# Performance work log

Hardware: AMD Instinct MI355X
Metric: run time of the kernel (lower is better)

The kernel has to match this reference:

```python
import math
import jax, jax.numpy as jnp
import numpy as np

N_HEADS = 16

def _alibi_slopes(n_heads: int) -> np.ndarray:
    def pow2_slopes(n):
        start = 2 ** (-2 ** (-(math.log2(n) - 3)))
        return [start * start ** i for i in range(n)]
    if math.log2(n_heads).is_integer():
        slopes = pow2_slopes(n_heads)
    else:
        closest = 2 ** math.floor(math.log2(n_heads))
        slopes = pow2_slopes(closest)
        extra = pow2_slopes(2 * closest)[0::2]
        slopes = slopes + extra[: n_heads - closest]
    return np.asarray(slopes, dtype=np.float32)

def _build_alibi_bias(n_heads: int, T: int) -> jnp.ndarray:
    # (1, H, T, T): lower triangle = -slope*|i-j|, strict upper = -inf (causal)
    slopes = jnp.asarray(_alibi_slopes(n_heads))  # (H,)
    pos = jnp.arange(T)
    dist = pos[None, :] - pos[None, :].T  # (T, T), j - i
    causal = dist < 0  # future positions (j > i means dist>0? note: dist = j - i transposed)
    # match torch: distances = positions[None,:] - positions[:,None] -> dist[i,j] = j - i
    dist = pos[None, :] - pos[:, None]
    causal = dist > 0  # wait: torch masks distances < 0 where distances[i,j] = j - i? No:
    # torch: distances = positions.unsqueeze(0) - positions.unsqueeze(1) -> dist[i,j] = positions[j] - positions[i]? 
    # unsqueeze(0): (1,T) row j; unsqueeze(1): (T,1) row i -> dist[i,j] = pos[j] - pos[i]
    # causal_mask = dist < 0 masks j < i ... but then bias upper triangle kept?
    # Actually torch masks where distances < 0, i.e., j < i (past). That seems inverted,
    # but we must be FAITHFUL: mask fills -inf where pos[j] - pos[i] < 0.
    d = pos[None, :] - pos[:, None]  # d[i,j] = j - i
    mask = d < 0
    bias = -slopes[:, None, None] * jnp.abs(d).astype(jnp.float32)[None, :, :]
    bias = jnp.where(mask[None, :, :], -jnp.inf, bias)
    return bias[None]  # (1, H, T, T)

def setup_inputs() -> dict:
    key = jax.random.key(0)
    k1, k2, k3 = jax.random.split(key, 3)
    B, T, D = 2, 2048, 1024
    x = jax.random.normal(k1, (B, T, D), dtype=jnp.float32)
    W_qkv = jax.random.normal(k2, (D, 3 * D), dtype=jnp.float32) * (1.0 / math.sqrt(D))
    W_out = jax.random.normal(k3, (D, D), dtype=jnp.float32) * (1.0 / math.sqrt(D))
    return {"x": x, "W_qkv": W_qkv, "W_out": W_out}

def reference(x, W_qkv, W_out):
    B, T, D = x.shape
    H = N_HEADS
    hd = D // H
    qkv = x @ W_qkv  # (B, T, 3D)
    q, k, v = jnp.split(qkv, 3, axis=-1)
    q = q.reshape(B, T, H, hd).transpose(0, 2, 1, 3)  # (B,H,T,hd)
    k = k.reshape(B, T, H, hd).transpose(0, 2, 1, 3)
    v = v.reshape(B, T, H, hd).transpose(0, 2, 1, 3)
    scale = 1.0 / math.sqrt(hd)
    attn = jnp.einsum('bhqd,bhkd->bhqk', q, k) * scale  # (B,H,T,T)
    attn = attn + _build_alibi_bias(H, T)
    attn = jax.nn.softmax(attn, axis=-1)
    out = jnp.einsum('bhqk,bhkd->bhqd', attn, v)  # (B,H,T,hd)
    out = out.transpose(0, 2, 1, 3).reshape(B, T, D)
    return out @ W_out
```

## Files before the change

kernel.cpp:

```cpp
#include <hip/hip_runtime.h>

#define DEV __device__ __forceinline__

typedef __attribute__((ext_vector_type(4))) float f32x4;
typedef __attribute__((ext_vector_type(16))) float f32x16;
typedef __attribute__((ext_vector_type(8))) short s16x8;

static constexpr int TB  = 2;
static constexpr int TT  = 2048;
static constexpr int TD  = 1024;
static constexpr int TH  = 16;
static constexpr int THD = 64;
static constexpr int TN3 = 3072;
static constexpr int TM  = TB * TT;

#define WS_XB     1024u
#define WS_WQKVT  (WS_XB + 8388608u)
#define WS_WOUTT  (WS_WQKVT + 6291456u)
#define WS_QKV    (WS_WOUTT + 2097152u)
#define WS_VT     (WS_QKV + 25165824u)
#define WS_CTX    (WS_VT + 8388608u)

DEV unsigned short f2bf(float f) {
  unsigned int u = __builtin_bit_cast(unsigned int, f);
  u += 0x7FFFu + ((u >> 16) & 1u);
  return (unsigned short)(u >> 16);
}
DEV f32x4 mfma16(s16x8 a, s16x8 b, f32x4 c) {
  return __builtin_amdgcn_mfma_f32_16x16x32_bf16(a, b, c, 0, 0, 0);
}
DEV f32x16 mfma32(s16x8 a, s16x8 b, f32x16 c) {
  return __builtin_amdgcn_mfma_f32_32x32x16_bf16(a, b, c, 0, 0, 0);
}
DEV void gload_lds16(const void* g, void* l) {
  __builtin_amdgcn_global_load_lds(
      (const __attribute__((address_space(1))) void*)g,
      (__attribute__((address_space(3))) void*)l, 16, 0, 0);
}
DEV unsigned int cvtpk(float lo, float hi_) {
  unsigned int r;
  asm("v_cvt_pk_bf16_f32 %0, %1, %2" : "=v"(r) : "v"(lo), "v"(hi_));
  return r;
}
DEV void plswap(unsigned int& a, unsigned int& b) {
  asm("v_permlane32_swap_b32 %0, %1" : "+v"(a), "+v"(b));
}

DEV bool is_bf16(const void* x) {
  uint4 v = ((const uint4*)x)[threadIdx.x & 63];
  unsigned int w[4] = {v.x, v.y, v.z, v.w};
  int hit = 0;
#pragma unroll
  for (int k = 0; k < 4; ++k) {
    if (((w[k] >> 7) & 0xFF) >= 135) hit++;
    if (((w[k] >> 23) & 0xFF) >= 135) hit++;
  }
  return __ballot(hit > 0) == 0ULL;
}

__global__ __launch_bounds__(256) void prep_kernel(const void* __restrict__ x,
                                                   const void* __restrict__ wqkv,
                                                   const void* __restrict__ wout,
                                                   unsigned short* __restrict__ xb,
                                                   unsigned short* __restrict__ wqkvt,
                                                   unsigned short* __restrict__ woutt) {
  __shared__ unsigned short tile[64 * 65];
  const int bid = blockIdx.x;
  const bool bf = is_bf16(x);
  if (bid < 1024) {
    const void* W; unsigned short* Wt; int N, k0, n0;
    if (bid < 768) { W = wqkv; Wt = wqkvt; N = TN3; k0 = (bid & 15) * 64; n0 = (bid >> 4) * 64; }
    else { int id = bid - 768; W = wout; Wt = woutt; N = TD; k0 = (id & 15) * 64; n0 = (id >> 4) * 64; }
    for (int e = threadIdx.x; e < 4096; e += 256) {
      int kr = e >> 6, nc = e & 63;
      unsigned short v;
      if (bf) v = ((const unsigned short*)W)[(size_t)(k0 + kr) * N + n0 + nc];
      else    v = f2bf(((const float*)W)[(size_t)(k0 + kr) * N + n0 + nc]);
      tile[kr * 65 + nc] = v;
    }
    __syncthreads();
    for (int e = threadIdx.x; e < 4096; e += 256) {
      int nr = e >> 6, kc = e & 63;
      Wt[(size_t)(n0 + nr) * TD + k0 + kc] = tile[kc * 65 + nr];
    }
  } else {
    if (bf) return;
    int i = (bid - 1024) * 256 + threadIdx.x;
    if (i >= (TM * TD) / 8) return;
    const float* s = (const float*)x + (size_t)i * 8;
    unsigned int w0 = (unsigned int)f2bf(s[0]) | ((unsigned int)f2bf(s[1]) << 16);
    unsigned int w1 = (unsigned int)f2bf(s[2]) | ((unsigned int)f2bf(s[3]) << 16);
    unsigned int w2 = (unsigned int)f2bf(s[4]) | ((unsigned int)f2bf(s[5]) << 16);
    unsigned int w3 = (unsigned int)f2bf(s[6]) | ((unsigned int)f2bf(s[7]) << 16);
    uint4 o; o.x = w0; o.y = w1; o.z = w2; o.w = w3;
    ((uint4*)xb)[i] = o;
  }
}

__global__ __launch_bounds__(512, 2) void gemm1_kernel(const unsigned short* __restrict__ Axb,
                                                       const unsigned short* __restrict__ xraw,
                                                       const unsigned short* __restrict__ Bt,
                                                       unsigned short* __restrict__ C,
                                                       unsigned short* __restrict__ vtb,
                                                       int Mn, int Nn, int Kn) {
  __shared__ unsigned short lA[2][256 * 64];
  __shared__ unsigned short lB[2][192 * 64];
  const int tid = threadIdx.x;
  const int lane = tid & 63;
  const int wid = tid >> 6;
  const int wm = wid >> 2, wn = wid & 3;
  const int l15 = lane & 15, lg = lane >> 4;

  const int nby = Nn / 192;
  const int nwg = (Mn >> 8) * nby;
  const int cpx = nwg >> 3;
  const int bid = blockIdx.x;
  const int swz = (bid & 7) * cpx + (bid >> 3);
  const int bm = swz / nby, bn = swz % nby;
  const int row0 = bm << 8, col0 = bn * 192;

  const bool bf = is_bf16(xraw);
  const unsigned short* Abase = bf ? xraw : Axb;

  const int srow = tid >> 3;
  const int scol = ((tid & 7) ^ (srow & 7)) * 8;
  const unsigned short* aS = Abase + (size_t)(row0 + srow) * Kn + scol;
  const unsigned short* bS = Bt + (size_t)(col0 + srow) * Kn + scol;
  const size_t r64 = (size_t)64 * Kn;

#define STGA(dst, koff) do {                                \
    unsigned short* _d = (dst) + tid * 8;                   \
    const unsigned short* _s = aS + (koff);                 \
    gload_lds16(_s,           _d);                          \
    gload_lds16(_s + r64,     _d + 4096);                   \
    gload_lds16(_s + 2 * r64, _d + 8192);                   \
    gload_lds16(_s + 3 * r64, _d + 12288);                  \
  } while (0)
#define STGB(dst, koff) do {                                \
    unsigned short* _d = (dst) + tid * 8;                   \
    const unsigned short* _s = bS + (koff);                 \
    gload_lds16(_s,           _d);                          \
    gload_lds16(_s + r64,     _d + 4096);                   \
    gload_lds16(_s + 2 * r64, _d + 8192);                   \
  } while (0)

  f32x4 acc[8][3];
#pragma unroll
  for (int m = 0; m < 8; ++m)
#pragma unroll
    for (int n = 0; n < 3; ++n) acc[m][n] = (f32x4){0.f, 0.f, 0.f, 0.f};

  const int sa = l15 & 7;
  const int kc0 = (lg ^ sa) * 8;
  const int kc1 = ((4 + lg) ^ sa) * 8;
  const int aRow = (wm * 128 + l15) * 64;
  const int bRow = (wn * 48 + l15) * 64;

  STGA(&lA[0][0], 0);
  STGB(&lB[0][0], 0);
  asm volatile("s_waitcnt vmcnt(0)" ::: "memory");
  __builtin_amdgcn_s_barrier();

  const int nt = Kn >> 6;
  for (int t = 0; t < nt; ++t) {
    const unsigned short* la = &lA[t & 1][0];
    const unsigned short* lb = &lB[t & 1][0];
    unsigned short* na = &lA[(t + 1) & 1][0];
    unsigned short* nb = &lB[(t + 1) & 1][0];
    const int koff = (t + 1) << 6;
    const bool more = (t + 1 < nt);

    s16x8 af[8], bv[3];

#pragma unroll
    for (int m = 0; m < 8; ++m) af[m] = *(const s16x8*)&la[aRow + m * 1024 + kc0];
#pragma unroll
    for (int n = 0; n < 3; ++n) bv[n] = *(const s16x8*)&lb[bRow + n * 1024 + kc0];
    if (more) STGA(na, koff);
    __builtin_amdgcn_s_barrier();
    asm volatile("s_waitcnt lgkmcnt(0)" ::: "memory");
    __builtin_amdgcn_sched_barrier(0);
    __builtin_amdgcn_s_setprio(1);
#pragma unroll
    for (int m = 0; m < 8; ++m)
#pragma unroll
      for (int n = 0; n < 3; ++n)
        acc[m][n] = mfma16(af[m], bv[n], acc[m][n]);
    __builtin_amdgcn_s_setprio(0);
    __builtin_amdgcn_s_barrier();

#pragma unroll
    for (int m = 0; m < 8; ++m) af[m] = *(const s16x8*)&la[aRow + m * 1024 + kc1];
#pragma unroll
    for (int n = 0; n < 3; ++n) bv[n] = *(const s16x8*)&lb[bRow + n * 1024 + kc1];
    if (more) STGB(nb, koff);
    __builtin_amdgcn_s_barrier();
    asm volatile("s_waitcnt lgkmcnt(0)" ::: "memory");
    __builtin_amdgcn_sched_barrier(0);
    __builtin_amdgcn_s_setprio(1);
#pragma unroll
    for (int m = 0; m < 8; ++m)
#pragma unroll
      for (int n = 0; n < 3; ++n)
        acc[m][n] = mfma16(af[m], bv[n], acc[m][n]);
    __builtin_amdgcn_s_setprio(0);
    asm volatile("s_waitcnt vmcnt(0)" ::: "memory");
    __builtin_amdgcn_s_barrier();
  }
#undef STGA
#undef STGB

  unsigned short* cw = C + (size_t)(row0 + wm * 128 + lg * 4) * Nn + col0 + wn * 48 + l15;
#pragma unroll
  for (int m = 0; m < 8; ++m)
#pragma unroll
    for (int n = 0; n < 3; ++n) {
      const int cbase = col0 + wn * 48 + n * 16;
      if (cbase < 2048) {
#pragma unroll
        for (int j = 0; j < 4; ++j)
          cw[(size_t)(m * 16 + j) * Nn + n * 16] = f2bf(acc[m][n][j]);
      } else {
        int tg = row0 + wm * 128 + lg * 4 + m * 16;
        int bb = tg >> 11, tt = tg & 2047;
        int cc2 = cbase + l15 - 2048;
        int h = cc2 >> 6, d = cc2 & 63;
        unsigned short* dst = vtb + (((size_t)(bb * 16 + h) * 64 + d) << 11) + tt;
        uint2 pk;
        pk.x = cvtpk(acc[m][n][0], acc[m][n][1]);
        pk.y = cvtpk(acc[m][n][2], acc[m][n][3]);
        *(uint2*)dst = pk;
      }
    }
}

__global__ __launch_bounds__(256, 2) void gemm_bt2_kernel(const unsigned short* __restrict__ A,
                                                          const unsigned short* __restrict__ Bt,
                                                          void* __restrict__ Cout,
                                                          int Mn, int Nn, int Kn,
                                                          const unsigned short* __restrict__ xprobe) {
  __shared__ unsigned short lA[3][128 * 64];
  __shared__ unsigned short lB[3][64 * 64];
  const int tid  = threadIdx.x;
  const int lane = tid & 63, wid = tid >> 6;
  const int wr = wid >> 1, wc = wid & 1;
  const int l15 = lane & 15, lg = lane >> 4;
  const int row0 = blockIdx.x * 128, col0 = blockIdx.y * 64;

  const bool obf = is_bf16(xprobe);

  f32x4 acc[4][2];
#pragma unroll
  for (int m = 0; m < 4; ++m)
#pragma unroll
    for (int n = 0; n < 2; ++n) acc[m][n] = (f32x4){0.f, 0.f, 0.f, 0.f};

  const int srow = tid >> 3;
  const int scol = ((tid & 7) ^ (srow & 7)) * 8;
  const unsigned short* aS = A  + (size_t)(row0 + srow) * Kn + scol;
  const unsigned short* bS = Bt + (size_t)(col0 + srow) * Kn + scol;
  const size_t r32 = (size_t)32 * Kn;

#define STG2(bi, koff) do {                                                 \
    unsigned short* _da = &lA[bi][0] + tid * 8;                             \
    unsigned short* _db = &lB[bi][0] + tid * 8;                             \
    gload_lds16(aS + (koff),            _da);                               \
    gload_lds16(aS + (koff) + r32,      _da + 2048);                        \
    gload_lds16(aS + (koff) + 2 * r32,  _da + 4096);                        \
    gload_lds16(aS + (koff) + 3 * r32,  _da + 6144);                        \
    gload_lds16(bS + (koff),            _db);                               \
    gload_lds16(bS + (koff) + r32,      _db + 2048);                        \
  } while (0)

  const int sa = l15 & 7;
  const int kc0 = (lg ^ sa) * 8;
  const int kc1 = ((4 + lg) ^ sa) * 8;
  const int aoff = (wr * 64 + l15) * 64;
  const int boff = (wc * 32 + l15) * 64;

  const int nt = Kn >> 6;
  STG2(0, 0);
  STG2(1, 64);
  asm volatile("s_waitcnt vmcnt(6)" ::: "memory");
  __builtin_amdgcn_s_barrier();

  int cur = 0;
  for (int t = 0; t < nt; ++t) {
    const unsigned short* la = &lA[cur][0];
    const unsigned short* lb = &lB[cur][0];
    const bool deep = (t + 2 < nt);

    s16x8 af[4], bfv[2];
#pragma unroll
    for (int m = 0; m < 4; ++m) af[m] = *(const s16x8*)&la[aoff + m * 1024 + kc0];
#pragma unroll
    for (int n = 0; n < 2; ++n) bfv[n] = *(const s16x8*)&lb[boff + n * 1024 + kc0];
    if (deep) { int nbuf = (cur + 2 == 3) ? 0 : ((cur + 2 == 4) ? 1 : cur + 2); STG2(nbuf, (t + 2) << 6); }
    __builtin_amdgcn_s_barrier();
    asm volatile("s_waitcnt lgkmcnt(0)" ::: "memory");
    __builtin_amdgcn_sched_barrier(0);
    __builtin_amdgcn_s_setprio(1);
#pragma unroll
    for (int m = 0; m < 4; ++m)
#pragma unroll
      for (int n = 0; n < 2; ++n)
        acc[m][n] = mfma16(af[m], bfv[n], acc[m][n]);
    __builtin_amdgcn_s_setprio(0);
    __builtin_amdgcn_s_barrier();

#pragma unroll
    for (int m = 0; m < 4; ++m) af[m] = *(const s16x8*)&la[aoff + m * 1024 + kc1];
#pragma unroll
    for (int n = 0; n < 2; ++n) bfv[n] = *(const s16x8*)&lb[boff + n * 1024 + kc1];
    __builtin_amdgcn_s_barrier();
    asm volatile("s_waitcnt lgkmcnt(0)" ::: "memory");
    __builtin_amdgcn_sched_barrier(0);
    __builtin_amdgcn_s_setprio(1);
#pragma unroll
    for (int m = 0; m < 4; ++m)
#pragma unroll
      for (int n = 0; n < 2; ++n)
        acc[m][n] = mfma16(af[m], bfv[n], acc[m][n]);
    __builtin_amdgcn_s_setprio(0);
    if (t + 1 < nt) {
      if (deep) asm volatile("s_waitcnt vmcnt(6)" ::: "memory");
      else      asm volatile("s_waitcnt vmcnt(0)" ::: "memory");
      __builtin_amdgcn_s_barrier();
    }
    cur = (cur == 2) ? 0 : cur + 1;
  }
#undef STG2

#pragma unroll
  for (int m = 0; m < 4; ++m)
#pragma unroll
    for (int n = 0; n < 2; ++n)
#pragma unroll
      for (int j = 0; j < 4; ++j) {
        int r = row0 + wr * 64 + m * 16 + lg * 4 + j;
        int c = col0 + wc * 32 + n * 16 + l15;
        if (obf) ((unsigned short*)Cout)[(size_t)r * Nn + c] = f2bf(acc[m][n][j]);
        else     ((float*)Cout)[(size_t)r * Nn + c] = acc[m][n][j];
      }
}

__global__ __launch_bounds__(256, 4) void attn_kernel(const unsigned short* __restrict__ qkv,
                                                      const unsigned short* __restrict__ vt,
                                                      unsigned short* __restrict__ ctx) {
  __shared__ __align__(16) unsigned char smem[32768];
  unsigned short* kl0 = (unsigned short*)smem;
  unsigned short* vl0 = (unsigned short*)(smem + 16384);
  float* red = (float*)smem;

  const int bid = blockIdx.x;
  const int q_ = bid >> 8;
  const int s_ = (bid >> 5) & 7;
  const int g_ = bid & 31;
  int bh, x32;
  if (q_ == 0)      { bh = g_;                   x32 = s_;      }
  else if (q_ == 1) { bh = g_ ^ 16;              x32 = 31 - s_; }
  else if (q_ == 2) { bh = (g_ + 8) & 31;        x32 = 15 - s_; }
  else              { bh = ((g_ + 8) & 31) ^ 16; x32 = 16 + s_; }
  const int b = bh >> 4, h = bh & 15;

  const int tid = threadIdx.x;
  const int wid = tid >> 6, lane = tid & 63;
  const int wr = wid & 1, wk = wid >> 1;
  const int l31 = lane & 31, hi = lane >> 5;
  const int i_base = x32 * 64 + wr * 32;

  const unsigned short* qb  = qkv + (size_t)b * TT * TN3 + h * THD;
  const unsigned short* kb_ = qkv + (size_t)b * TT * TN3 + TD + h * THD;
  const unsigned short* vb_ = vt + (size_t)bh * THD * TT;

  const float LOG2E = 1.44269504f;
  const float SL2 = exp2f(-0.5f * (float)(h + 1)) * LOG2E;
  const float SC2 = 0.125f * LOG2E;
  const float dbias = -SL2 * 64.0f;

  const int t_rel = (int)((40.0f / SL2 + 63.0f) * (1.0f / 64.0f)) + 1;
  const int t_end = (32 < x32 + t_rel) ? 32 : x32 + t_rel;

  const int srow = tid >> 3;
  const int sx = ((tid & 7) ^ (srow & 7)) * 8;
  const unsigned short* srcK = kb_ + (size_t)(x32 * 64 + srow) * TN3 + sx;
  const unsigned short* srcV = vb_ + (size_t)srow * TT + x32 * 64 + sx;
  const size_t kstep = (size_t)64 * TN3;

#define STAGE(bufi) do {                                   \
    unsigned short* _dk = kl0 + (bufi) * 4096 + tid * 8;   \
    unsigned short* _dv = vl0 + (bufi) * 4096 + tid * 8;   \
    gload_lds16(srcK,            _dk);                     \
    gload_lds16(srcK + 32 * TN3, _dk + 2048);              \
    gload_lds16(srcV,            _dv);                     \
    gload_lds16(srcV + 32 * TT,  _dv + 2048);              \
  } while (0)

  s16x8 qa[4];
  {
    const unsigned short* qr = qb + (size_t)(i_base + l31) * TN3 + hi * 8;
#pragma unroll
    for (int dd = 0; dd < 4; ++dd) qa[dd] = *(const s16x8*)(qr + dd * 16);
  }

  s16x8 ones;
  {
    short ov = (l31 == 0) ? (short)0x3F80 : (short)0;
#pragma unroll
    for (int e = 0; e < 8; ++e) ones[e] = ov;
  }

  float base[16];
#pragma unroll
  for (int r = 0; r < 16; ++r) {
    int cr0 = (r & 3) + 8 * (r >> 2);
    base[r] = -SL2 * (float)(wk * 32 + cr0 + 4 * hi - wr * 32 - l31) - 16.0f;
  }

  f32x16 o0, o1, ol;
#pragma unroll
  for (int r = 0; r < 16; ++r) { o0[r] = 0.f; o1[r] = 0.f; ol[r] = 0.f; }

  const int sw = (l31 & 7) << 4;
  int cc[4];
#pragma unroll
  for (int dd = 0; dd < 4; ++dd) cc[dd] = ((dd * 32 + hi * 16) ^ sw) >> 1;

  int cur = 0;
  STAGE(0); srcK += kstep; srcV += 64;
  asm volatile("s_waitcnt vmcnt(0)" ::: "memory");
  __syncthreads();

  for (int t = x32; t < t_end; ++t) {
    if (t + 1 < t_end) { STAGE(cur ^ 1); srcK += kstep; srcV += 64; }

    const unsigned short* kb = kl0 + cur * 4096;
    const unsigned short* vbl = vl0 + cur * 4096;

    f32x16 sv;
#pragma unroll
    for (int r = 0; r < 16; ++r) sv[r] = 0.f;
    __builtin_amdgcn_s_setprio(1);
#pragma unroll
    for (int dd = 0; dd < 4; ++dd) {
      s16x8 k0 = *(const s16x8*)&kb[(wk * 32 + l31) * 64 + cc[dd]];
      sv = mfma32(k0, qa[dd], sv);
    }
    __builtin_amdgcn_s_setprio(0);

    if (t == x32) {
#pragma unroll
      for (int r = 0; r < 16; ++r) {
        float bb = base[r];
        float v = __builtin_amdgcn_exp2f(fmaf(sv[r], SC2, bb));
        sv[r] = (bb > -15.999f) ? 0.0f : v;
      }
    } else {
#pragma unroll
      for (int r = 0; r < 16; ++r)
        sv[r] = __builtin_amdgcn_exp2f(fmaf(sv[r], SC2, base[r]));
    }
#pragma unroll
    for (int r = 0; r < 16; ++r) base[r] += dbias;

    s16x8 pa[2];
#pragma unroll
    for (int mh = 0; mh < 2; ++mh) {
      unsigned int a0 = cvtpk(sv[8 * mh + 0], sv[8 * mh + 1]);
      unsigned int a1 = cvtpk(sv[8 * mh + 2], sv[8 * mh + 3]);
      unsigned int b0 = cvtpk(sv[8 * mh + 4], sv[8 * mh + 5]);
      unsigned int b1 = cvtpk(sv[8 * mh + 6], sv[8 * mh + 7]);
      plswap(a0, b0); plswap(a1, b1);
      uint4 u; u.x = a0; u.y = a1; u.z = b0; u.w = b1;
      pa[mh] = __builtin_bit_cast(s16x8, u);
    }

    __builtin_amdgcn_s_setprio(1);
#pragma unroll
    for (int ks = 0; ks < 2; ++ks) {
      s16x8 v0 = *(const s16x8*)&vbl[l31 * 64 + cc[wk * 2 + ks]];
      s16x8 v1 = *(const s16x8*)&vbl[(32 + l31) * 64 + cc[wk * 2 + ks]];
      o0 = mfma32(pa[ks], v0, o0);
      o1 = mfma32(pa[ks], v1, o1);
      ol = mfma32(pa[ks], ones, ol);
    }
    __builtin_amdgcn_s_setprio(0);

    asm volatile("s_waitcnt vmcnt(0)" ::: "memory");
    __syncthreads();
    cur ^= 1;
  }
#undef STAGE

  const int rbase = (wr * 64 + lane) * 49;
  if (wk == 1) {
#pragma unroll
    for (int r = 0; r < 16; ++r) red[rbase + r] = o0[r];
#pragma unroll
    for (int r = 0; r < 16; ++r) red[rbase + 16 + r] = o1[r];
#pragma unroll
    for (int r = 0; r < 16; ++r) red[rbase + 32 + r] = ol[r];
  }
  __syncthreads();
  if (wk == 0) {
#pragma unroll
    for (int r = 0; r < 16; ++r) o0[r] += red[rbase + r];
#pragma unroll
    for (int r = 0; r < 16; ++r) o1[r] += red[rbase + 16 + r];
#pragma unroll
    for (int r = 0; r < 16; ++r) ol[r] += red[rbase + 32 + r];

    float rdiv[16];
#pragma unroll
    for (int r = 0; r < 16; ++r) rdiv[r] = 1.0f / __shfl(ol[r], lane & 32);

    unsigned short* cb = ctx + (size_t)(b * TT + i_base) * TD + h * THD + l31;
#pragma unroll
    for (int r = 0; r < 16; ++r) {
      int row = (r & 3) + 8 * (r >> 2) + 4 * hi;
      unsigned int pk = cvtpk(o0[r] * rdiv[r], o1[r] * rdiv[r]);
      cb[(size_t)row * TD] = (unsigned short)pk;
      cb[(size_t)row * TD + 32] = (unsigned short)(pk >> 16);
    }
  }
}

extern "C" void kernel_launch(void* const* d_in, const int* in_sizes, int n_in,
                              void* d_out, int out_size, void* d_ws, size_t ws_size,
                              hipStream_t stream) {
  const void* x    = d_in[0];
  const void* wqkv = d_in[1];
  const void* wout = d_in[2];
  char* ws = (char*)d_ws;
  unsigned short* xb    = (unsigned short*)(ws + WS_XB);
  unsigned short* wqkvt = (unsigned short*)(ws + WS_WQKVT);
  unsigned short* woutt = (unsigned short*)(ws + WS_WOUTT);
  unsigned short* qkvb  = (unsigned short*)(ws + WS_QKV);
  unsigned short* vtb   = (unsigned short*)(ws + WS_VT);
  unsigned short* ctxb  = (unsigned short*)(ws + WS_CTX);

  prep_kernel<<<3072, 256, 0, stream>>>(x, wqkv, wout, xb, wqkvt, woutt);
  gemm1_kernel<<<(TM / 256) * (TN3 / 192), 512, 0, stream>>>(xb, (const unsigned short*)x, wqkvt, qkvb, vtb, TM, TN3, TD);
  attn_kernel<<<1024, 256, 0, stream>>>(qkvb, vtb, ctxb);
  gemm_bt2_kernel<<<dim3(TM / 128, TD / 64), 256, 0, stream>>>(ctxb, woutt, d_out, TM, TD, TD, (const unsigned short*)x);
}
```

Baseline: 94.50 us.

## Restructure QKV GEMM pipeline with combined staging and partial vmcnt waits; remap attention blocks

The QKV GEMM main loop now issues the B-tile and A-tile global-to-LDS loads together at the start of each iteration. It splits compute by M halves, each half covering the full K=64 step, instead of by K halves. Partial vmcnt waits replace the full drain, so later loads can still be in flight while earlier MFMAs run. The attention kernel's block-to-(batch, head, query tile) mapping is changed to pair heads h and 15-h across passes, which aims to balance per-block work given ALiBi-dependent key-range truncation. The vmcnt counts rely on a precise load ordering and risk races if miscounted.

```diff
diff --git a/kernel.cpp b/kernel.cpp
--- a/kernel.cpp
+++ b/kernel.cpp
@@ -128,20 +128,18 @@
   const unsigned short* bS = Bt + (size_t)(col0 + srow) * Kn + scol;
   const size_t r64 = (size_t)64 * Kn;
 
-#define STGA(dst, koff) do {                                \
-    unsigned short* _d = (dst) + tid * 8;                   \
-    const unsigned short* _s = aS + (koff);                 \
-    gload_lds16(_s,           _d);                          \
-    gload_lds16(_s + r64,     _d + 4096);                   \
-    gload_lds16(_s + 2 * r64, _d + 8192);                   \
-    gload_lds16(_s + 3 * r64, _d + 12288);                  \
-  } while (0)
-#define STGB(dst, koff) do {                                \
-    unsigned short* _d = (dst) + tid * 8;                   \
-    const unsigned short* _s = bS + (koff);                 \
-    gload_lds16(_s,           _d);                          \
-    gload_lds16(_s + r64,     _d + 4096);                   \
-    gload_lds16(_s + 2 * r64, _d + 8192);                   \
+#define STG_ORD(dst_a, dst_b, koff) do {                    \
+    const unsigned short* _sa = aS + (koff);                \
+    const unsigned short* _sb = bS + (koff);                \
+    unsigned short* _da = (dst_a) + tid * 8;                \
+    unsigned short* _db = (dst_b) + tid * 8;                \
+    gload_lds16(_sb,           _db);                        \
+    gload_lds16(_sb + r64,     _db + 4096);                 \
+    gload_lds16(_sb + 2 * r64, _db + 8192);                 \
+    gload_lds16(_sa,           _da);                        \
+    gload_lds16(_sa + 2 * r64, _da + 8192);                 \
+    gload_lds16(_sa + r64,     _da + 4096);                 \
+    gload_lds16(_sa + 3 * r64, _da + 12288);                \
   } while (0)
 
   f32x4 acc[8][3];
@@ -156,9 +154,8 @@
   const int aRow = (wm * 128 + l15) * 64;
   const int bRow = (wn * 48 + l15) * 64;
 
-  STGA(&lA[0][0], 0);
-  STGB(&lB[0][0], 0);
-  asm volatile("s_waitcnt vmcnt(0)" ::: "memory");
+  STG_ORD(&lA[0][0], &lB[0][0], 0);
+  asm volatile("s_waitcnt vmcnt(2)" ::: "memory");
   __builtin_amdgcn_s_barrier();
 
   const int nt = Kn >> 6;
@@ -170,45 +167,56 @@
     const int koff = (t + 1) << 6;
     const bool more = (t + 1 < nt);
 
-    s16x8 af[8], bv[3];
-
-#pragma unroll
-    for (int m = 0; m < 8; ++m) af[m] = *(const s16x8*)&la[aRow + m * 1024 + kc0];
-#pragma unroll
-    for (int n = 0; n < 3; ++n) bv[n] = *(const s16x8*)&lb[bRow + n * 1024 + kc0];
-    if (more) STGA(na, koff);
+    s16x8 af[4][2], bv[3][2];
+
+#pragma unroll
+    for (int m = 0; m < 4; ++m) {
+      af[m][0] = *(const s16x8*)&la[aRow + m * 1024 + kc0];
+      af[m][1] = *(const s16x8*)&la[aRow + m * 1024 + kc1];
+    }
+#pragma unroll
+    for (int n = 0; n < 3; ++n) {
+      bv[n][0] = *(const s16x8*)&lb[bRow + n * 1024 + kc0];
+      bv[n][1] = *(const s16x8*)&lb[bRow + n * 1024 + kc1];
+    }
+    if (more) STG_ORD(na, nb, koff);
     __builtin_amdgcn_s_barrier();
     asm volatile("s_waitcnt lgkmcnt(0)" ::: "memory");
     __builtin_amdgcn_sched_barrier(0);
     __builtin_amdgcn_s_setprio(1);
 #pragma unroll
-    for (int m = 0; m < 8; ++m)
-#pragma unroll
-      for (int n = 0; n < 3; ++n)
-        acc[m][n] = mfma16(af[m], bv[n], acc[m][n]);
+    for (int m = 0; m < 4; ++m)
+#pragma unroll
+      for (int n = 0; n < 3; ++n) {
+        acc[m][n] = mfma16(af[m][0], bv[n][0], acc[m][n]);
+        acc[m][n] = mfma16(af[m][1], bv[n][1], acc[m][n]);
+      }
     __builtin_amdgcn_s_setprio(0);
-    __builtin_amdgcn_s_barrier();
-
-#pragma unroll
-    for (int m = 0; m < 8; ++m) af[m] = *(const s16x8*)&la[aRow + m * 1024 + kc1];
-#pragma unroll
-    for (int n = 0; n < 3; ++n) bv[n] = *(const s16x8*)&lb[bRow + n * 1024 + kc1];
-    if (more) STGB(nb, koff);
+    if (more) asm volatile("s_waitcnt vmcnt(7)" ::: "memory");
+    else      asm volatile("s_waitcnt vmcnt(0)" ::: "memory");
+    __builtin_amdgcn_s_barrier();
+
+#pragma unroll
+    for (int m = 0; m < 4; ++m) {
+      af[m][0] = *(const s16x8*)&la[aRow + (4 + m) * 1024 + kc0];
+      af[m][1] = *(const s16x8*)&la[aRow + (4 + m) * 1024 + kc1];
+    }
     __builtin_amdgcn_s_barrier();
     asm volatile("s_waitcnt lgkmcnt(0)" ::: "memory");
     __builtin_amdgcn_sched_barrier(0);
     __builtin_amdgcn_s_setprio(1);
 #pragma unroll
-    for (int m = 0; m < 8; ++m)
-#pragma unroll
-      for (int n = 0; n < 3; ++n)
-        acc[m][n] = mfma16(af[m], bv[n], acc[m][n]);
+    for (int m = 0; m < 4; ++m)
+#pragma unroll
+      for (int n = 0; n < 3; ++n) {
+        acc[4 + m][n] = mfma16(af[m][0], bv[n][0], acc[4 + m][n]);
+        acc[4 + m][n] = mfma16(af[m][1], bv[n][1], acc[4 + m][n]);
+      }
     __builtin_amdgcn_s_setprio(0);
-    asm volatile("s_waitcnt vmcnt(0)" ::: "memory");
-    __builtin_amdgcn_s_barrier();
-  }
-#undef STGA
-#undef STGB
+    if (more) asm volatile("s_waitcnt vmcnt(2)" ::: "memory");
+    __builtin_amdgcn_s_barrier();
+  }
+#undef STG_ORD
 
   unsigned short* cw = C + (size_t)(row0 + wm * 128 + lg * 4) * Nn + col0 + wn * 48 + l15;
 #pragma unroll
@@ -353,15 +361,17 @@
   float* red = (float*)smem;
 
   const int bid = blockIdx.x;
-  const int q_ = bid >> 8;
+  const int p_ = bid >> 8;
   const int s_ = (bid >> 5) & 7;
   const int g_ = bid & 31;
-  int bh, x32;
-  if (q_ == 0)      { bh = g_;                   x32 = s_;      }
-  else if (q_ == 1) { bh = g_ ^ 16;              x32 = 31 - s_; }
-  else if (q_ == 2) { bh = (g_ + 8) & 31;        x32 = 15 - s_; }
-  else              { bh = ((g_ + 8) & 31) ^ 16; x32 = 16 + s_; }
-  const int b = bh >> 4, h = bh & 15;
+  const int hh = g_ & 15, bb_ = g_ >> 4;
+  int h_, x32;
+  if (p_ == 0)      { h_ = hh;      x32 = s_;      }
+  else if (p_ == 1) { h_ = hh;      x32 = 31 - s_; }
+  else if (p_ == 2) { h_ = 15 - hh; x32 = 15 - s_; }
+  else              { h_ = 15 - hh; x32 = 16 + s_; }
+  const int bh = bb_ * 16 + h_;
+  const int b = bb_, h = h_;
 
   const int tid = threadIdx.x;
   const int wid = tid >> 6, lane = tid & 63;
```

After: 94.91 us. About the same (+0.4%).
